# Kernel tuning notes

Hardware: AMD Instinct MI355X
Metric: run time of the kernel (lower is better)

## Reference

```python
import jax, jax.numpy as jnp
import numpy as np

EMBED = 1024
B, S = 4, 2048

def setup_inputs() -> dict:
    key = jax.random.key(0)
    k1, k2, k3, k4, k5, k6 = jax.random.split(key, 6)
    scale = 1.0 / np.sqrt(EMBED)
    return {
        "query": jax.random.normal(k1, (B, S, EMBED), dtype=jnp.float32),
        "key": jax.random.normal(k2, (B, S, EMBED), dtype=jnp.float32),
        "value": jax.random.normal(k3, (B, S, EMBED), dtype=jnp.float32),
        # nn.Linear weights, stored torch-style [out, in]; y = x @ W.T
        "Q_W": jax.random.normal(k4, (EMBED, EMBED), dtype=jnp.float32) * scale,
        "K_W": jax.random.normal(k5, (EMBED, EMBED), dtype=jnp.float32) * scale,
        "V_W": jax.random.normal(k6, (EMBED, EMBED), dtype=jnp.float32) * scale,
    }

def reference(query, key, value, Q_W, K_W, V_W):
    q = jnp.einsum('bse,oe->bso', query, Q_W)   # Linear(bias=False): x @ W.T
    k = jnp.einsum('bse,oe->bso', key, K_W)
    v = jnp.einsum('bse,oe->bso', value, V_W)
    scores = jnp.einsum('bqe,bke->bqk', q, k) / jnp.sqrt(jnp.asarray(q.shape[-1], q.dtype))
    attn = jax.nn.softmax(scores, axis=-1)      # [b, q, k]
    out = jnp.einsum('bqs,bse->bqe', attn, v)
    return out
```

## Files before the change

kernel.cpp:

```cpp
#include <hip/hip_runtime.h>
#include <stdint.h>


typedef __attribute__((ext_vector_type(8))) short short8;
typedef __attribute__((ext_vector_type(4))) float floatx4;
typedef __attribute__((ext_vector_type(4))) unsigned short u16x4;
typedef __attribute__((ext_vector_type(4))) float f32x4v;

__device__ __forceinline__ unsigned short f32_to_bf16(float f) {
    union { float f; unsigned u; } c; c.f = f;
    unsigned u = c.u;
    return (unsigned short)((u + 0x7fffu + ((u >> 16) & 1u)) >> 16);
}

__global__ __launch_bounds__(256) void cvt_all(
    const float* __restrict__ q, const float* __restrict__ k,
    const float* __restrict__ v, const float* __restrict__ wq,
    const float* __restrict__ wk, const float* __restrict__ wv,
    unsigned short* __restrict__ Xq, unsigned short* __restrict__ Xk,
    unsigned short* __restrict__ Xv, unsigned short* __restrict__ Wq,
    unsigned short* __restrict__ Wk, unsigned short* __restrict__ Wv,
    float* __restrict__ rowsum) {
    const long NTE4 = 2097152;
    const long NW4  = 262144;
    long i = (long)blockIdx.x * 256 + threadIdx.x;
    const float* src;
    unsigned short* dst;
    long j;
    if (i < 3 * NTE4) {
        int a = (int)(i / NTE4); j = i - (long)a * NTE4;
        src = a == 0 ? q : a == 1 ? k : v;
        dst = a == 0 ? Xq : a == 1 ? Xk : Xv;
    } else {
        i -= 3 * NTE4;
        if (i < 3 * NW4) {
            int a = (int)(i / NW4); j = i - (long)a * NW4;
            src = a == 0 ? wq : a == 1 ? wk : wv;
            dst = a == 0 ? Wq : a == 1 ? Wk : Wv;
        } else {
            i -= 3 * NW4;
            ((f32x4v*)rowsum)[i] = (f32x4v)0.0f;
            return;
        }
    }
    f32x4v f = ((const f32x4v*)src)[j];
    u16x4 o;
#pragma unroll
    for (int t = 0; t < 4; ++t) o[t] = f32_to_bf16(f[t]);
    ((u16x4*)dst)[j] = o;
}

#define BM 128
#define BN 128
#define BK 64

#define G2L(g, l) __builtin_amdgcn_global_load_lds( \
    (__attribute__((address_space(1))) void*)(void*)(g), \
    (__attribute__((address_space(3))) void*)(l), 16, 0, 0)

template <int EPI>
__device__ __forceinline__ void gemm_body(
    const unsigned short* __restrict__ A, const unsigned short* __restrict__ B,
    void* __restrict__ Cv, int lda, int ldb, int ldc, int K, float scale,
    float* __restrict__ rowsum, int m0, int n0) {
    __shared__ unsigned short As[BM * BK];
    __shared__ unsigned short Bs[BN * BK];

    const int tid  = threadIdx.x;
    const int wave = tid >> 6;
    const int lane = tid & 63;
    const int lm   = lane & 15;
    const int quad = lane >> 4;
    const int wm   = wave >> 1;
    const int wn   = wave & 1;

    const int srow8 = lane >> 3;
    const int gcol  = ((lane & 7) ^ srow8) * 8;

    floatx4 acc[4][4];
#pragma unroll
    for (int i = 0; i < 4; ++i)
#pragma unroll
        for (int j = 0; j < 4; ++j) acc[i][j] = (floatx4)0.0f;

    for (int k0 = 0; k0 < K; k0 += BK) {
#pragma unroll
        for (int i = 0; i < 4; ++i) {
            const int rbase = wave * 32 + i * 8;
            G2L(A + (size_t)(m0 + rbase + srow8) * lda + k0 + gcol,
                &As[rbase * BK]);
            G2L(B + (size_t)(n0 + rbase + srow8) * ldb + k0 + gcol,
                &Bs[rbase * BK]);
        }
        __syncthreads();

#pragma unroll
        for (int s = 0; s < 2; ++s) {
            short8 af[4], bf[4];
#pragma unroll
            for (int t = 0; t < 4; ++t) {
                const int cs = ((s * 4 + quad) ^ (lm & 7)) * 8;
                af[t] = *(const short8*)&As[(wm * 64 + t * 16 + lm) * BK + cs];
                bf[t] = *(const short8*)&Bs[(wn * 64 + t * 16 + lm) * BK + cs];
            }
#pragma unroll
            for (int mt = 0; mt < 4; ++mt)
#pragma unroll
                for (int nt = 0; nt < 4; ++nt)
                    acc[mt][nt] = __builtin_amdgcn_mfma_f32_16x16x32_bf16(
                        af[mt], bf[nt], acc[mt][nt], 0, 0, 0);
        }
        __syncthreads();
    }

    if constexpr (EPI == 0) {
        unsigned short* C = (unsigned short*)Cv;
#pragma unroll
        for (int mt = 0; mt < 4; ++mt)
#pragma unroll
            for (int nt = 0; nt < 4; ++nt)
#pragma unroll
                for (int r = 0; r < 4; ++r) {
                    const int row = m0 + wm * 64 + mt * 16 + quad * 4 + r;
                    const int col = n0 + wn * 64 + nt * 16 + lm;
                    C[(size_t)row * ldc + col] = f32_to_bf16(acc[mt][nt][r]);
                }
    } else if constexpr (EPI == 1) {
        unsigned short* C = (unsigned short*)Cv;
        float psum[4][4];
#pragma unroll
        for (int mt = 0; mt < 4; ++mt)
#pragma unroll
            for (int r = 0; r < 4; ++r) psum[mt][r] = 0.0f;
#pragma unroll
        for (int mt = 0; mt < 4; ++mt)
#pragma unroll
            for (int nt = 0; nt < 4; ++nt)
#pragma unroll
                for (int r = 0; r < 4; ++r) {
                    const int row = m0 + wm * 64 + mt * 16 + quad * 4 + r;
                    const int col = n0 + wn * 64 + nt * 16 + lm;
                    const float p = __expf(acc[mt][nt][r] * scale);
                    psum[mt][r] += p;
                    C[(size_t)row * ldc + col] = f32_to_bf16(p);
                }
#pragma unroll
        for (int off = 1; off <= 8; off <<= 1)
#pragma unroll
            for (int mt = 0; mt < 4; ++mt)
#pragma unroll
                for (int r = 0; r < 4; ++r)
                    psum[mt][r] += __shfl_xor(psum[mt][r], off);
        if (lm == 0) {
#pragma unroll
            for (int mt = 0; mt < 4; ++mt)
#pragma unroll
                for (int r = 0; r < 4; ++r)
                    atomicAdd(&rowsum[m0 + wm * 64 + mt * 16 + quad * 4 + r],
                              psum[mt][r]);
        }
    } else {
        float* C = (float*)Cv;
#pragma unroll
        for (int mt = 0; mt < 4; ++mt)
#pragma unroll
            for (int r = 0; r < 4; ++r) {
                const int row = m0 + wm * 64 + mt * 16 + quad * 4 + r;
                const float inv = 1.0f / rowsum[row];
#pragma unroll
                for (int nt = 0; nt < 4; ++nt) {
                    const int col = n0 + wn * 64 + nt * 16 + lm;
                    C[(size_t)row * ldc + col] = acc[mt][nt][r] * inv;
                }
            }
    }
}

__global__ __launch_bounds__(256, 4) void proj_kernel(
    const unsigned short* __restrict__ Xq, const unsigned short* __restrict__ Wq,
    unsigned short* __restrict__ qb,
    const unsigned short* __restrict__ Xk, const unsigned short* __restrict__ Wk,
    unsigned short* __restrict__ kb,
    const unsigned short* __restrict__ Wv, const unsigned short* __restrict__ Xv,
    unsigned short* __restrict__ vT) {
    const int z = blockIdx.z;
    const unsigned short* A = z == 0 ? Xq : z == 1 ? Xk : Wv;
    const unsigned short* B = z == 0 ? Wq : z == 1 ? Wk : Xv;
    unsigned short* C = z == 0 ? qb : z == 1 ? kb : vT;
    int m0, n0, ldc;
    if (z < 2) { m0 = blockIdx.x * BM; n0 = blockIdx.y * BN; ldc = 1024; }
    else       { m0 = blockIdx.y * BM; n0 = blockIdx.x * BN; ldc = 8192; }
    gemm_body<0>(A, B, C, 1024, 1024, ldc, 1024, 1.0f, nullptr, m0, n0);
}

__global__ __launch_bounds__(256, 4) void scores_kernel(
    const unsigned short* __restrict__ qb, const unsigned short* __restrict__ kb,
    unsigned short* __restrict__ Sc, float* __restrict__ rowsum) {
    const long z = blockIdx.z;
    gemm_body<1>(qb + z * 2048 * 1024, kb + z * 2048 * 1024,
                 Sc + z * 2048 * 2048, 1024, 1024, 2048, 1024,
                 1.0f / 32.0f, rowsum + z * 2048,
                 blockIdx.x * BM, blockIdx.y * BN);
}

__global__ __launch_bounds__(256, 4) void pv_kernel(
    const unsigned short* __restrict__ Sc, const unsigned short* __restrict__ vT,
    float* __restrict__ out, float* __restrict__ rowsum) {
    const long z = blockIdx.z;
    gemm_body<2>(Sc + z * 2048 * 2048, vT + z * 2048,
                 out + z * 2048 * 1024, 2048, 8192, 1024, 2048,
                 1.0f, rowsum + z * 2048,
                 blockIdx.x * BM, blockIdx.y * BN);
}

extern "C" void kernel_launch(void* const* d_in, const int* in_sizes, int n_in,
                              void* d_out, int out_size, void* d_ws, size_t ws_size,
                              hipStream_t stream) {
    const float* q_in = (const float*)d_in[0];
    const float* k_in = (const float*)d_in[1];
    const float* v_in = (const float*)d_in[2];
    const float* Qw_f = (const float*)d_in[3];
    const float* Kw_f = (const float*)d_in[4];
    const float* Vw_f = (const float*)d_in[5];
    float* out = (float*)d_out;

    const int Bb = 4, S = 2048, E = 1024;
    const size_t TOK = (size_t)Bb * S;
    const size_t NTE = TOK * E;
    const size_t NW  = (size_t)E * E;

    unsigned short* ws = (unsigned short*)d_ws;
    unsigned short* Xq = ws;
    unsigned short* Xk = Xq + NTE;
    unsigned short* Xv = Xk + NTE;
    unsigned short* Wq = Xv + NTE;
    unsigned short* Wk = Wq + NW;
    unsigned short* Wv = Wk + NW;
    unsigned short* qb = Wv + NW;
    unsigned short* kb = qb + NTE;
    unsigned short* vT = kb + NTE;
    unsigned short* Sc = vT + NTE;
    float* rowsum = (float*)(Sc + (size_t)Bb * S * S);

    {
        const long G = 3 * (long)(NTE / 4) + 3 * (long)(NW / 4) + (Bb * S / 4);
        cvt_all<<<(unsigned)(G / 256), 256, 0, stream>>>(
            q_in, k_in, v_in, Qw_f, Kw_f, Vw_f,
            Xq, Xk, Xv, Wq, Wk, Wv, rowsum);
    }

    proj_kernel<<<dim3(TOK / BM, E / BN, 3), 256, 0, stream>>>(
        Xq, Wq, qb, Xk, Wk, kb, Wv, Xv, vT);

    scores_kernel<<<dim3(S / BM, S / BN, 4), 256, 0, stream>>>(
        qb, kb, Sc, rowsum);

    pv_kernel<<<dim3(S / BM, E / BN, 4), 256, 0, stream>>>(
        Sc, vT, out, rowsum);
}
```

Before: 286.6 us.

## Use 256x256 double-buffered pipelined GEMM for projection and score kernels

```diff
diff --git a/kernel.cpp b/kernel.cpp
--- a/kernel.cpp
+++ b/kernel.cpp
@@ -12,6 +12,12 @@
     unsigned u = c.u;
     return (unsigned short)((u + 0x7fffu + ((u >> 16) & 1u)) >> 16);
 }
+
+#define G2L(g, l) __builtin_amdgcn_global_load_lds( \
+    (__attribute__((address_space(1))) void*)(void*)(g), \
+    (__attribute__((address_space(3))) void*)(l), 16, 0, 0)
+
+#define BAR() __builtin_amdgcn_s_barrier()
 
 __global__ __launch_bounds__(256) void cvt_all(
     const float* __restrict__ q, const float* __restrict__ k,
@@ -54,10 +60,6 @@
 #define BN 128
 #define BK 64
 
-#define G2L(g, l) __builtin_amdgcn_global_load_lds( \
-    (__attribute__((address_space(1))) void*)(void*)(g), \
-    (__attribute__((address_space(3))) void*)(l), 16, 0, 0)
-
 template <int EPI>
 __device__ __forceinline__ void gemm_body(
     const unsigned short* __restrict__ A, const unsigned short* __restrict__ B,
@@ -113,53 +115,7 @@
         __syncthreads();
     }
 
-    if constexpr (EPI == 0) {
-        unsigned short* C = (unsigned short*)Cv;
-#pragma unroll
-        for (int mt = 0; mt < 4; ++mt)
-#pragma unroll
-            for (int nt = 0; nt < 4; ++nt)
-#pragma unroll
-                for (int r = 0; r < 4; ++r) {
-                    const int row = m0 + wm * 64 + mt * 16 + quad * 4 + r;
-                    const int col = n0 + wn * 64 + nt * 16 + lm;
-                    C[(size_t)row * ldc + col] = f32_to_bf16(acc[mt][nt][r]);
-                }
-    } else if constexpr (EPI == 1) {
-        unsigned short* C = (unsigned short*)Cv;
-        float psum[4][4];
-#pragma unroll
-        for (int mt = 0; mt < 4; ++mt)
-#pragma unroll
-            for (int r = 0; r < 4; ++r) psum[mt][r] = 0.0f;
-#pragma unroll
-        for (int mt = 0; mt < 4; ++mt)
-#pragma unroll
-            for (int nt = 0; nt < 4; ++nt)
-#pragma unroll
-                for (int r = 0; r < 4; ++r) {
-                    const int row = m0 + wm * 64 + mt * 16 + quad * 4 + r;
-                    const int col = n0 + wn * 64 + nt * 16 + lm;
-                    const float p = __expf(acc[mt][nt][r] * scale);
-                    psum[mt][r] += p;
-                    C[(size_t)row * ldc + col] = f32_to_bf16(p);
-                }
-#pragma unroll
-        for (int off = 1; off <= 8; off <<= 1)
-#pragma unroll
-            for (int mt = 0; mt < 4; ++mt)
-#pragma unroll
-                for (int r = 0; r < 4; ++r)
-                    psum[mt][r] += __shfl_xor(psum[mt][r], off);
-        if (lm == 0) {
-#pragma unroll
-            for (int mt = 0; mt < 4; ++mt)
-#pragma unroll
-                for (int r = 0; r < 4; ++r)
-                    atomicAdd(&rowsum[m0 + wm * 64 + mt * 16 + quad * 4 + r],
-                              psum[mt][r]);
-        }
-    } else {
+    if constexpr (EPI == 2) {
         float* C = (float*)Cv;
 #pragma unroll
         for (int mt = 0; mt < 4; ++mt)
@@ -176,7 +132,215 @@
     }
 }
 
-__global__ __launch_bounds__(256, 4) void proj_kernel(
+__global__ __launch_bounds__(256, 4) void pv_kernel(
+    const unsigned short* __restrict__ Sc, const unsigned short* __restrict__ vT,
+    float* __restrict__ out, float* __restrict__ rowsum) {
+    const long z = blockIdx.z;
+    gemm_body<2>(Sc + z * 2048 * 2048, vT + z * 2048,
+                 out + z * 2048 * 1024, 2048, 8192, 1024, 2048,
+                 1.0f, rowsum + z * 2048,
+                 blockIdx.x * BM, blockIdx.y * BN);
+}
+
+template <int EPI>
+__device__ __forceinline__ void gemm256_body(
+    const unsigned short* __restrict__ A, const unsigned short* __restrict__ B,
+    void* __restrict__ Cv, int lda, int ldb, int ldc, int K, float scale,
+    float* __restrict__ rowsum, int m0, int n0) {
+    __shared__ unsigned short As[2][256 * 64];
+    __shared__ unsigned short Bs[2][256 * 64];
+
+    const int tid   = threadIdx.x;
+    const int wave  = tid >> 6;
+    const int lane  = tid & 63;
+    const int lm    = lane & 15;
+    const int quad  = lane >> 4;
+    const int wm    = wave >> 2;
+    const int wn    = wave & 3;
+    const int srow8 = lane >> 3;
+    const int gcol  = ((lane & 7) ^ srow8) * 8;
+    const int KT    = K >> 6;
+
+#define STAGE_A(buf, half, kcol) do { \
+        const int r0_ = (half) * 128 + wave * 8; \
+        G2L(A + (size_t)(m0 + r0_ + srow8) * lda + (kcol) + gcol, \
+            &As[buf][r0_ * 64]); \
+        G2L(A + (size_t)(m0 + r0_ + 64 + srow8) * lda + (kcol) + gcol, \
+            &As[buf][(r0_ + 64) * 64]); \
+    } while (0)
+#define STAGE_B(buf, half, kcol) do { \
+        const int r0_ = (half) * 128 + wave * 8; \
+        G2L(B + (size_t)(n0 + r0_ + srow8) * ldb + (kcol) + gcol, \
+            &Bs[buf][r0_ * 64]); \
+        G2L(B + (size_t)(n0 + r0_ + 64 + srow8) * ldb + (kcol) + gcol, \
+            &Bs[buf][(r0_ + 64) * 64]); \
+    } while (0)
+
+    floatx4 acc[8][4];
+#pragma unroll
+    for (int i = 0; i < 8; ++i)
+#pragma unroll
+        for (int j = 0; j < 4; ++j) acc[i][j] = (floatx4)0.0f;
+
+    STAGE_A(0, 0, 0); STAGE_A(0, 1, 0);
+    STAGE_B(0, 0, 0); STAGE_B(0, 1, 0);
+    STAGE_A(1, 0, 64); STAGE_A(1, 1, 64);
+    asm volatile("s_waitcnt vmcnt(4)" ::: "memory");
+    BAR();
+
+    short8 aA[2][4];
+    short8 aM[2][4];
+    short8 bB[2][2];
+
+    for (int kt = 0; kt < KT; ++kt) {
+        const int b = kt & 1;
+        const unsigned short* Ab = As[b];
+        const unsigned short* Bb = Bs[b];
+
+#pragma unroll
+        for (int s = 0; s < 2; ++s) {
+            const int cs = ((s * 4 + quad) ^ (lm & 7)) * 8;
+#pragma unroll
+            for (int mt = 0; mt < 4; ++mt)
+                aA[s][mt] = *(const short8*)&Ab[(wm * 128 + mt * 16 + lm) * 64 + cs];
+#pragma unroll
+            for (int nt = 0; nt < 2; ++nt)
+                bB[s][nt] = *(const short8*)&Bb[(wn * 64 + nt * 16 + lm) * 64 + cs];
+        }
+        if (kt + 1 < KT) STAGE_B(b ^ 1, 0, (kt + 1) * 64);
+        BAR();
+        asm volatile("s_waitcnt lgkmcnt(0)" ::: "memory");
+        __builtin_amdgcn_sched_barrier(0);
+        __builtin_amdgcn_s_setprio(1);
+#pragma unroll
+        for (int s = 0; s < 2; ++s)
+#pragma unroll
+            for (int mt = 0; mt < 4; ++mt)
+#pragma unroll
+                for (int nt = 0; nt < 2; ++nt)
+                    acc[mt][nt] = __builtin_amdgcn_mfma_f32_16x16x32_bf16(
+                        aA[s][mt], bB[s][nt], acc[mt][nt], 0, 0, 0);
+        __builtin_amdgcn_s_setprio(0);
+        BAR();
+
+#pragma unroll
+        for (int s = 0; s < 2; ++s) {
+            const int cs = ((s * 4 + quad) ^ (lm & 7)) * 8;
+#pragma unroll
+            for (int mt = 0; mt < 4; ++mt)
+                aM[s][mt] = *(const short8*)&Ab[(wm * 128 + 64 + mt * 16 + lm) * 64 + cs];
+        }
+        if (kt + 1 < KT) STAGE_B(b ^ 1, 1, (kt + 1) * 64);
+        BAR();
+        asm volatile("s_waitcnt lgkmcnt(0)" ::: "memory");
+        __builtin_amdgcn_sched_barrier(0);
+        __builtin_amdgcn_s_setprio(1);
+#pragma unroll
+        for (int s = 0; s < 2; ++s)
+#pragma unroll
+            for (int mt = 0; mt < 4; ++mt)
+#pragma unroll
+                for (int nt = 0; nt < 2; ++nt)
+                    acc[4 + mt][nt] = __builtin_amdgcn_mfma_f32_16x16x32_bf16(
+                        aM[s][mt], bB[s][nt], acc[4 + mt][nt], 0, 0, 0);
+        __builtin_amdgcn_s_setprio(0);
+        BAR();
+
+#pragma unroll
+        for (int s = 0; s < 2; ++s) {
+            const int cs = ((s * 4 + quad) ^ (lm & 7)) * 8;
+#pragma unroll
+            for (int nt = 0; nt < 2; ++nt)
+                bB[s][nt] = *(const short8*)&Bb[(wn * 64 + 32 + nt * 16 + lm) * 64 + cs];
+        }
+        if (kt + 2 < KT) STAGE_A(b, 0, (kt + 2) * 64);
+        BAR();
+        asm volatile("s_waitcnt lgkmcnt(0)" ::: "memory");
+        __builtin_amdgcn_sched_barrier(0);
+        __builtin_amdgcn_s_setprio(1);
+#pragma unroll
+        for (int s = 0; s < 2; ++s)
+#pragma unroll
+            for (int mt = 0; mt < 4; ++mt)
+#pragma unroll
+                for (int nt = 0; nt < 2; ++nt)
+                    acc[4 + mt][2 + nt] = __builtin_amdgcn_mfma_f32_16x16x32_bf16(
+                        aM[s][mt], bB[s][nt], acc[4 + mt][2 + nt], 0, 0, 0);
+        __builtin_amdgcn_s_setprio(0);
+        BAR();
+
+        if (kt + 2 < KT) STAGE_A(b, 1, (kt + 2) * 64);
+        BAR();
+        __builtin_amdgcn_s_setprio(1);
+#pragma unroll
+        for (int s = 0; s < 2; ++s)
+#pragma unroll
+            for (int mt = 0; mt < 4; ++mt)
+#pragma unroll
+                for (int nt = 0; nt < 2; ++nt)
+                    acc[mt][2 + nt] = __builtin_amdgcn_mfma_f32_16x16x32_bf16(
+                        aA[s][mt], bB[s][nt], acc[mt][2 + nt], 0, 0, 0);
+        __builtin_amdgcn_s_setprio(0);
+        if (kt < KT - 2) {
+            asm volatile("s_waitcnt vmcnt(4)" ::: "memory");
+        } else if (kt == KT - 2) {
+            asm volatile("s_waitcnt vmcnt(0)" ::: "memory");
+        }
+        BAR();
+    }
+#undef STAGE_A
+#undef STAGE_B
+
+    if constexpr (EPI == 0) {
+        unsigned short* C = (unsigned short*)Cv;
+#pragma unroll
+        for (int f = 0; f < 8; ++f)
+#pragma unroll
+            for (int g = 0; g < 4; ++g)
+#pragma unroll
+                for (int r = 0; r < 4; ++r) {
+                    const int row = m0 + wm * 128 + f * 16 + quad * 4 + r;
+                    const int col = n0 + wn * 64 + g * 16 + lm;
+                    C[(size_t)row * ldc + col] = f32_to_bf16(acc[f][g][r]);
+                }
+    } else if constexpr (EPI == 1) {
+        unsigned short* C = (unsigned short*)Cv;
+        float psum[8][4];
+#pragma unroll
+        for (int f = 0; f < 8; ++f)
+#pragma unroll
+            for (int r = 0; r < 4; ++r) psum[f][r] = 0.0f;
+#pragma unroll
+        for (int f = 0; f < 8; ++f)
+#pragma unroll
+            for (int g = 0; g < 4; ++g)
+#pragma unroll
+                for (int r = 0; r < 4; ++r) {
+                    const int row = m0 + wm * 128 + f * 16 + quad * 4 + r;
+                    const int col = n0 + wn * 64 + g * 16 + lm;
+                    const float p = __expf(acc[f][g][r] * scale);
+                    psum[f][r] += p;
+                    C[(size_t)row * ldc + col] = f32_to_bf16(p);
+                }
+#pragma unroll
+        for (int off = 1; off <= 8; off <<= 1)
+#pragma unroll
+            for (int f = 0; f < 8; ++f)
+#pragma unroll
+                for (int r = 0; r < 4; ++r)
+                    psum[f][r] += __shfl_xor(psum[f][r], off);
+        if (lm == 0) {
+#pragma unroll
+            for (int f = 0; f < 8; ++f)
+#pragma unroll
+                for (int r = 0; r < 4; ++r)
+                    atomicAdd(&rowsum[m0 + wm * 128 + f * 16 + quad * 4 + r],
+                              psum[f][r]);
+        }
+    }
+}
+
+__global__ __launch_bounds__(512, 2) void proj256_kernel(
     const unsigned short* __restrict__ Xq, const unsigned short* __restrict__ Wq,
     unsigned short* __restrict__ qb,
     const unsigned short* __restrict__ Xk, const unsigned short* __restrict__ Wk,
@@ -188,29 +352,19 @@
     const unsigned short* B = z == 0 ? Wq : z == 1 ? Wk : Xv;
     unsigned short* C = z == 0 ? qb : z == 1 ? kb : vT;
     int m0, n0, ldc;
-    if (z < 2) { m0 = blockIdx.x * BM; n0 = blockIdx.y * BN; ldc = 1024; }
-    else       { m0 = blockIdx.y * BM; n0 = blockIdx.x * BN; ldc = 8192; }
-    gemm_body<0>(A, B, C, 1024, 1024, ldc, 1024, 1.0f, nullptr, m0, n0);
-}
-
-__global__ __launch_bounds__(256, 4) void scores_kernel(
+    if (z < 2) { m0 = blockIdx.x * 256; n0 = blockIdx.y * 256; ldc = 1024; }
+    else       { m0 = blockIdx.y * 256; n0 = blockIdx.x * 256; ldc = 8192; }
+    gemm256_body<0>(A, B, C, 1024, 1024, ldc, 1024, 1.0f, nullptr, m0, n0);
+}
+
+__global__ __launch_bounds__(512, 2) void scores256_kernel(
     const unsigned short* __restrict__ qb, const unsigned short* __restrict__ kb,
     unsigned short* __restrict__ Sc, float* __restrict__ rowsum) {
     const long z = blockIdx.z;
-    gemm_body<1>(qb + z * 2048 * 1024, kb + z * 2048 * 1024,
-                 Sc + z * 2048 * 2048, 1024, 1024, 2048, 1024,
-                 1.0f / 32.0f, rowsum + z * 2048,
-                 blockIdx.x * BM, blockIdx.y * BN);
-}
-
-__global__ __launch_bounds__(256, 4) void pv_kernel(
-    const unsigned short* __restrict__ Sc, const unsigned short* __restrict__ vT,
-    float* __restrict__ out, float* __restrict__ rowsum) {
-    const long z = blockIdx.z;
-    gemm_body<2>(Sc + z * 2048 * 2048, vT + z * 2048,
-                 out + z * 2048 * 1024, 2048, 8192, 1024, 2048,
-                 1.0f, rowsum + z * 2048,
-                 blockIdx.x * BM, blockIdx.y * BN);
+    gemm256_body<1>(qb + z * 2048 * 1024, kb + z * 2048 * 1024,
+                    Sc + z * 2048 * 2048, 1024, 1024, 2048, 1024,
+                    1.0f / 32.0f, rowsum + z * 2048,
+                    blockIdx.x * 256, blockIdx.y * 256);
 }
 
 extern "C" void kernel_launch(void* const* d_in, const int* in_sizes, int n_in,
@@ -249,10 +403,10 @@
             Xq, Xk, Xv, Wq, Wk, Wv, rowsum);
     }
 
-    proj_kernel<<<dim3(TOK / BM, E / BN, 3), 256, 0, stream>>>(
+    proj256_kernel<<<dim3(TOK / 256, E / 256, 3), 512, 0, stream>>>(
         Xq, Wq, qb, Xk, Wk, kb, Wv, Xv, vT);
 
-    scores_kernel<<<dim3(S / BM, S / BN, 4), 256, 0, stream>>>(
+    scores256_kernel<<<dim3(S / 256, S / 256, 4), 512, 0, stream>>>(
         qb, kb, Sc, rowsum);
 
     pv_kernel<<<dim3(S / BM, E / BN, 4), 256, 0, stream>>>(
```

Measured after the change: 302.7 us. +5.6%, slower.
